# Performance work log

Measured on AMD Instinct MI355X. Metric: run time of the kernel, lower is better.

## Reference

```python
import jax, jax.numpy as jnp
import numpy as np

B = 8192
D_IN = 512
UNITS = 512


def setup_inputs() -> dict:
    key = jax.random.key(0)
    ks = jax.random.split(key, 9)
    sx = 1.0 / np.sqrt(D_IN)
    sh = 1.0 / np.sqrt(UNITS)
    return {
        "input_x": jax.random.normal(ks[0], (B, D_IN), jnp.float32),
        "input_h": jax.random.normal(ks[1], (B, UNITS), jnp.float32),
        "attention_score": jax.random.uniform(ks[2], (B, 1), jnp.float32),
        "Wx_r": jax.random.normal(ks[3], (D_IN, UNITS), jnp.float32) * sx,
        "b_r": jnp.zeros((UNITS,), jnp.float32),
        "Wh_r": jax.random.normal(ks[4], (UNITS, UNITS), jnp.float32) * sh,
        "Wx_u": jax.random.normal(ks[5], (D_IN, UNITS), jnp.float32) * sx,
        "b_u": jnp.zeros((UNITS,), jnp.float32),
        "Wh_u": jax.random.normal(ks[6], (UNITS, UNITS), jnp.float32) * sh,
        "Wx_h": jax.random.normal(ks[7], (D_IN, UNITS), jnp.float32) * sx,
        "b_h": jnp.zeros((UNITS,), jnp.float32),
        "Wh_h": jax.random.normal(ks[8], (UNITS, UNITS), jnp.float32) * sh,
    }


def reference(input_x, input_h, attention_score,
              Wx_r, b_r, Wh_r,
              Wx_u, b_u, Wh_u,
              Wx_h, b_h, Wh_h):
    # reset gate: sigmoid(Dense_b(x) + Dense(h))
    r = jax.nn.sigmoid(input_x @ Wx_r + b_r + input_h @ Wh_r)
    # update gate: sigmoid(Dense_b(x) + Dense(h))
    u = jax.nn.sigmoid(input_x @ Wx_u + b_u + input_h @ Wh_u)
    # candidate: tanh(Dense_b(x) + r * Dense(h))
    cal_h = jnp.tanh(input_x @ Wx_h + b_h + r * (input_h @ Wh_h))
    # attention-modulated update and interpolation
    u_att = attention_score * u
    h = (1.0 - u_att) * input_h + u_att * cal_h
    return h
```

## Files before the change

kernel.cpp:

```cpp
#include <hip/hip_runtime.h>
#include <hip/hip_bf16.h>

typedef __bf16 bf16x8 __attribute__((ext_vector_type(8)));
typedef float f32x4 __attribute__((ext_vector_type(4)));
typedef unsigned short us8 __attribute__((ext_vector_type(8)));

#define MFMA16 __builtin_amdgcn_mfma_f32_16x16x32_bf16

__device__ __forceinline__ unsigned short f2bf(float f) {
    unsigned int u = __float_as_uint(f);
    u += 0x7fffu + ((u >> 16) & 1u);
    return (unsigned short)(u >> 16);
}

__device__ __forceinline__ void gload_lds16(const void* g, void* l) {
    __builtin_amdgcn_global_load_lds(
        (const __attribute__((address_space(1))) unsigned int*)g,
        (__attribute__((address_space(3))) unsigned int*)l, 16, 0, 0);
}

__global__ void cvt_all_kernel(const float* __restrict__ x, const float* __restrict__ h,
                               unsigned short* __restrict__ XP, unsigned short* __restrict__ HP,
                               const float* __restrict__ W0, const float* __restrict__ W1,
                               const float* __restrict__ W2, const float* __restrict__ W3,
                               const float* __restrict__ W4, const float* __restrict__ W5,
                               unsigned short* __restrict__ WP) {
    if (blockIdx.x < 4096) {
        int c = blockIdx.x * 256 + threadIdx.x;
        const float* src = (c >> 19) ? h : x;
        unsigned short* dst = (c >> 19) ? HP : XP;
        int c2 = c & 524287;
        int mb = c2 >> 10, kb = (c2 >> 6) & 15, lane = c2 & 63;
        int r = lane & 15, ko = lane >> 4;
        const float* p = src + (size_t)(mb * 16 + r) * 512 + kb * 32 + ko * 8;
        float4 v0 = *(const float4*)p;
        float4 v1 = *(const float4*)(p + 4);
        us8 o = { f2bf(v0.x), f2bf(v0.y), f2bf(v0.z), f2bf(v0.w),
                  f2bf(v1.x), f2bf(v1.y), f2bf(v1.z), f2bf(v1.w) };
        *(us8*)(dst + (size_t)c2 * 8) = o;
    } else {
        int c = (blockIdx.x - 4096) * 256 + threadIdx.x;
        int w = c >> 15;
        const float* Wsrc;
        switch (w) {
            case 0: Wsrc = W0; break;
            case 1: Wsrc = W1; break;
            case 2: Wsrc = W2; break;
            case 3: Wsrc = W3; break;
            case 4: Wsrc = W4; break;
            default: Wsrc = W5; break;
        }
        int c2 = c & 32767;
        int nb = c2 >> 10, kb = (c2 >> 6) & 15, lane = c2 & 63;
        int cc = lane & 15, ko = lane >> 4;
        int kbase = kb * 32 + ko * 8;
        us8 o;
#pragma unroll
        for (int e = 0; e < 8; ++e)
            o[e] = f2bf(Wsrc[(size_t)(kbase + e) * 512 + nb * 16 + cc]);
        *(us8*)(WP + (size_t)c * 8) = o;
    }
}

__global__ __launch_bounds__(512, 4) void augru_mm(
    const unsigned short* __restrict__ XP,
    const unsigned short* __restrict__ HP,
    const unsigned short* __restrict__ WP,
    const float* __restrict__ b_r, const float* __restrict__ b_u, const float* __restrict__ b_h,
    const float* __restrict__ att, const float* __restrict__ h32,
    float* __restrict__ out) {
    __shared__ unsigned char sB[48 * 1024];

    const int t = threadIdx.x;
    const int wv = t >> 6, lane = t & 63;
    const int laneoff = lane * 16;

    const int bid = blockIdx.x;
    const int W = (bid & 7) * 64 + (bid >> 3);
    const int mblk = W >> 4, nblk = W & 15;
    const int wr = wv >> 1, wc = wv & 1;

    f32x4 accR[4] = {}, accU[4] = {}, accXH[4] = {}, accHH[4] = {};

    const unsigned char* XPb = (const unsigned char*)XP;
    const unsigned char* HPb = (const unsigned char*)HP;
    const unsigned char* WPb = (const unsigned char*)WP;

    size_t aoff[4];
#pragma unroll
    for (int mf = 0; mf < 4; ++mf)
        aoff[mf] = ((size_t)((mblk * 16 + wr * 4 + mf) * 16) << 10) + laneoff;

    const unsigned char* wsrc[6];
    unsigned sdst[6];
#pragma unroll
    for (int i = 0; i < 6; ++i) {
        int fid = wv + i * 8;
        int s = fid >> 3, nf = (fid >> 2) & 1, kbi = fid & 3;
        wsrc[i] = WPb + ((size_t)(s * 512 + (nblk * 2 + nf) * 16 + kbi) << 10) + laneoff;
        sdst[i] = (unsigned)fid << 10;
    }

#pragma unroll
    for (int c = 0; c < 4; ++c) {
        __syncthreads();
#pragma unroll
        for (int i = 0; i < 6; ++i)
            gload_lds16(wsrc[i] + ((size_t)c << 12), &sB[sdst[i]]);
        __syncthreads();

#pragma unroll
        for (int kbi = 0; kbi < 4; ++kbi) {
            const int kb = c * 4 + kbi;
            const size_t koff = (size_t)kb << 10;
            bf16x8 ax[4], ah[4];
#pragma unroll
            for (int mf = 0; mf < 4; ++mf) ax[mf] = *(const bf16x8*)(XPb + aoff[mf] + koff);
            const unsigned rb = (unsigned)((wc * 4 + kbi) << 10) + laneoff;
            bf16x8 b0 = *(const bf16x8*)&sB[0 * 8192 + rb];
            bf16x8 b2 = *(const bf16x8*)&sB[2 * 8192 + rb];
            bf16x8 b4 = *(const bf16x8*)&sB[4 * 8192 + rb];
#pragma unroll
            for (int mf = 0; mf < 4; ++mf) ah[mf] = *(const bf16x8*)(HPb + aoff[mf] + koff);
            __builtin_amdgcn_s_setprio(1);
#pragma unroll
            for (int mf = 0; mf < 4; ++mf) {
                accR[mf]  = MFMA16(ax[mf], b0, accR[mf], 0, 0, 0);
                accU[mf]  = MFMA16(ax[mf], b2, accU[mf], 0, 0, 0);
                accXH[mf] = MFMA16(ax[mf], b4, accXH[mf], 0, 0, 0);
            }
            __builtin_amdgcn_s_setprio(0);
            bf16x8 b1 = *(const bf16x8*)&sB[1 * 8192 + rb];
            bf16x8 b3 = *(const bf16x8*)&sB[3 * 8192 + rb];
            bf16x8 b5 = *(const bf16x8*)&sB[5 * 8192 + rb];
            __builtin_amdgcn_s_setprio(1);
#pragma unroll
            for (int mf = 0; mf < 4; ++mf) {
                accR[mf]  = MFMA16(ah[mf], b1, accR[mf], 0, 0, 0);
                accU[mf]  = MFMA16(ah[mf], b3, accU[mf], 0, 0, 0);
                accHH[mf] = MFMA16(ah[mf], b5, accHH[mf], 0, 0, 0);
            }
            __builtin_amdgcn_s_setprio(0);
        }
    }

    const int lr = lane & 15, lg = lane >> 4;
    const int col = nblk * 32 + wc * 16 + lr;
    const float br = b_r[col], bu = b_u[col], bh = b_h[col];
#pragma unroll
    for (int mf = 0; mf < 4; ++mf) {
        const int rowb = mblk * 256 + wr * 64 + mf * 16 + lg * 4;
#pragma unroll
        for (int q = 0; q < 4; ++q) {
            const int row = rowb + q;
            float r = 1.f / (1.f + __expf(-(accR[mf][q] + br)));
            float u = 1.f / (1.f + __expf(-(accU[mf][q] + bu)));
            float ph = accXH[mf][q] + bh + r * accHH[mf][q];
            ph = fminf(fmaxf(ph, -15.f), 15.f);
            float e = __expf(2.f * ph);
            float cal = (e - 1.f) / (e + 1.f);
            float hv = h32[(size_t)row * 512 + col];
            float ua = att[row] * u;
            out[(size_t)row * 512 + col] = fmaf(ua, cal - hv, hv);
        }
    }
}

extern "C" void kernel_launch(void* const* d_in, const int* in_sizes, int n_in,
                              void* d_out, int out_size, void* d_ws, size_t ws_size,
                              hipStream_t stream) {
    const float* x    = (const float*)d_in[0];
    const float* h    = (const float*)d_in[1];
    const float* att  = (const float*)d_in[2];
    const float* Wx_r = (const float*)d_in[3];
    const float* b_r  = (const float*)d_in[4];
    const float* Wh_r = (const float*)d_in[5];
    const float* Wx_u = (const float*)d_in[6];
    const float* b_u  = (const float*)d_in[7];
    const float* Wh_u = (const float*)d_in[8];
    const float* Wx_h = (const float*)d_in[9];
    const float* b_h  = (const float*)d_in[10];
    const float* Wh_h = (const float*)d_in[11];
    float* out = (float*)d_out;

    unsigned short* XP = (unsigned short*)d_ws;
    unsigned short* HP = XP + 8192 * 512;
    unsigned short* WP = HP + 8192 * 512;

    cvt_all_kernel<<<4864, 256, 0, stream>>>(x, h, XP, HP,
        Wx_r, Wh_r, Wx_u, Wh_u, Wx_h, Wh_h, WP);
    augru_mm<<<512, 512, 0, stream>>>(XP, HP, WP, b_r, b_u, b_h, att, h, out);
}
```

Baseline: 52.41 us.

## Concatenate x|h along K and double-buffer A and W tiles in LDS

The converter now packs x and h into one concatenated [B, 1024] bf16 fragment layout, and the weights into matching per-gate K-concatenated fragments. The GEMM kernel uses 256x64 output tiles instead of 256x32, so it launches 256 blocks. It stages both A and B tiles into two LDS buffers with async global-to-LDS loads and explicit vmcnt waits and barriers, replacing the previous direct global reads of A. This doubles B-fragment reuse per A load and overlaps the next tile's loads with MFMA work. In exchange it uses about 112KB of LDS and twice the accumulators per thread, which lowers occupancy, and it fills only 256 blocks.

```diff
diff --git a/kernel.cpp b/kernel.cpp
--- a/kernel.cpp
+++ b/kernel.cpp
@@ -20,15 +20,15 @@
 }
 
 __global__ void cvt_all_kernel(const float* __restrict__ x, const float* __restrict__ h,
-                               unsigned short* __restrict__ XP, unsigned short* __restrict__ HP,
+                               unsigned short* __restrict__ AP,
                                const float* __restrict__ W0, const float* __restrict__ W1,
                                const float* __restrict__ W2, const float* __restrict__ W3,
                                const float* __restrict__ W4, const float* __restrict__ W5,
                                unsigned short* __restrict__ WP) {
     if (blockIdx.x < 4096) {
         int c = blockIdx.x * 256 + threadIdx.x;
-        const float* src = (c >> 19) ? h : x;
-        unsigned short* dst = (c >> 19) ? HP : XP;
+        int ih = c >> 19;
+        const float* src = ih ? h : x;
         int c2 = c & 524287;
         int mb = c2 >> 10, kb = (c2 >> 6) & 15, lane = c2 & 63;
         int r = lane & 15, ko = lane >> 4;
@@ -37,133 +37,148 @@
         float4 v1 = *(const float4*)(p + 4);
         us8 o = { f2bf(v0.x), f2bf(v0.y), f2bf(v0.z), f2bf(v0.w),
                   f2bf(v1.x), f2bf(v1.y), f2bf(v1.z), f2bf(v1.w) };
-        *(us8*)(dst + (size_t)c2 * 8) = o;
+        *((us8*)AP + ((size_t)(mb * 32 + kb + ih * 16) << 6) + lane) = o;
     } else {
         int c = (blockIdx.x - 4096) * 256 + threadIdx.x;
-        int w = c >> 15;
+        int s = c >> 16, c2 = c & 65535;
+        int frag = c2 >> 6, lane = c2 & 63;
+        int nb = frag >> 5, kbp = frag & 31;
         const float* Wsrc;
-        switch (w) {
-            case 0: Wsrc = W0; break;
-            case 1: Wsrc = W1; break;
-            case 2: Wsrc = W2; break;
-            case 3: Wsrc = W3; break;
-            case 4: Wsrc = W4; break;
-            default: Wsrc = W5; break;
-        }
-        int c2 = c & 32767;
-        int nb = c2 >> 10, kb = (c2 >> 6) & 15, lane = c2 & 63;
+        int kb;
+        if (kbp < 16) { kb = kbp;      Wsrc = (s == 0) ? W0 : (s == 1) ? W2 : W4; }
+        else          { kb = kbp - 16; Wsrc = (s == 0) ? W1 : (s == 1) ? W3 : W5; }
         int cc = lane & 15, ko = lane >> 4;
         int kbase = kb * 32 + ko * 8;
         us8 o;
 #pragma unroll
         for (int e = 0; e < 8; ++e)
             o[e] = f2bf(Wsrc[(size_t)(kbase + e) * 512 + nb * 16 + cc]);
-        *(us8*)(WP + (size_t)c * 8) = o;
-    }
-}
-
-__global__ __launch_bounds__(512, 4) void augru_mm(
-    const unsigned short* __restrict__ XP,
-    const unsigned short* __restrict__ HP,
-    const unsigned short* __restrict__ WP,
+        *((us8*)WP + c) = o;
+    }
+}
+
+__global__ __launch_bounds__(512, 2) void augru_mm(
+    const unsigned short* __restrict__ AP_,
+    const unsigned short* __restrict__ WP_,
     const float* __restrict__ b_r, const float* __restrict__ b_u, const float* __restrict__ b_h,
     const float* __restrict__ att, const float* __restrict__ h32,
     float* __restrict__ out) {
-    __shared__ unsigned char sB[48 * 1024];
-
-    const int t = threadIdx.x;
-    const int wv = t >> 6, lane = t & 63;
+    __shared__ unsigned char sL[2][57344];
+    const unsigned char* AP  = (const unsigned char*)AP_;
+    const unsigned char* WPb = (const unsigned char*)WP_;
+
+    const int t = threadIdx.x, wv = t >> 6, lane = t & 63;
     const int laneoff = lane * 16;
 
     const int bid = blockIdx.x;
-    const int W = (bid & 7) * 64 + (bid >> 3);
-    const int mblk = W >> 4, nblk = W & 15;
+    const int Wid = (bid & 7) * 32 + (bid >> 3);
+    const int mblk = Wid >> 3, nblk = Wid & 7;
     const int wr = wv >> 1, wc = wv & 1;
 
-    f32x4 accR[4] = {}, accU[4] = {}, accXH[4] = {}, accHH[4] = {};
-
-    const unsigned char* XPb = (const unsigned char*)XP;
-    const unsigned char* HPb = (const unsigned char*)HP;
-    const unsigned char* WPb = (const unsigned char*)WP;
-
-    size_t aoff[4];
-#pragma unroll
-    for (int mf = 0; mf < 4; ++mf)
-        aoff[mf] = ((size_t)((mblk * 16 + wr * 4 + mf) * 16) << 10) + laneoff;
-
-    const unsigned char* wsrc[6];
-    unsigned sdst[6];
-#pragma unroll
-    for (int i = 0; i < 6; ++i) {
-        int fid = wv + i * 8;
-        int s = fid >> 3, nf = (fid >> 2) & 1, kbi = fid & 3;
-        wsrc[i] = WPb + ((size_t)(s * 512 + (nblk * 2 + nf) * 16 + kbi) << 10) + laneoff;
-        sdst[i] = (unsigned)fid << 10;
-    }
-
-#pragma unroll
-    for (int c = 0; c < 4; ++c) {
-        __syncthreads();
-#pragma unroll
-        for (int i = 0; i < 6; ++i)
-            gload_lds16(wsrc[i] + ((size_t)c << 12), &sB[sdst[i]]);
-        __syncthreads();
-
-#pragma unroll
-        for (int kbi = 0; kbi < 4; ++kbi) {
-            const int kb = c * 4 + kbi;
-            const size_t koff = (size_t)kb << 10;
-            bf16x8 ax[4], ah[4];
-#pragma unroll
-            for (int mf = 0; mf < 4; ++mf) ax[mf] = *(const bf16x8*)(XPb + aoff[mf] + koff);
-            const unsigned rb = (unsigned)((wc * 4 + kbi) << 10) + laneoff;
-            bf16x8 b0 = *(const bf16x8*)&sB[0 * 8192 + rb];
-            bf16x8 b2 = *(const bf16x8*)&sB[2 * 8192 + rb];
-            bf16x8 b4 = *(const bf16x8*)&sB[4 * 8192 + rb];
-#pragma unroll
-            for (int mf = 0; mf < 4; ++mf) ah[mf] = *(const bf16x8*)(HPb + aoff[mf] + koff);
-            __builtin_amdgcn_s_setprio(1);
-#pragma unroll
-            for (int mf = 0; mf < 4; ++mf) {
-                accR[mf]  = MFMA16(ax[mf], b0, accR[mf], 0, 0, 0);
-                accU[mf]  = MFMA16(ax[mf], b2, accU[mf], 0, 0, 0);
-                accXH[mf] = MFMA16(ax[mf], b4, accXH[mf], 0, 0, 0);
+    f32x4 accR[4][2] = {}, accU[4][2] = {}, accXH[4][2] = {}, accHH[4][2] = {};
+
+    const unsigned char* gsrc[7];
+    unsigned ldst[7];
+#pragma unroll
+    for (int i = 0; i < 4; ++i) {
+        int f = i * 8 + wv, mbL = f >> 1, kq = f & 1;
+        gsrc[i] = AP + ((size_t)((mblk * 16 + mbL) * 32 + kq) << 10) + laneoff;
+        ldst[i] = (unsigned)f << 10;
+    }
+#pragma unroll
+    for (int i = 4; i < 7; ++i) {
+        int g = (i - 4) * 8 + wv, s = g >> 3, nbL = (g >> 1) & 3, kq = g & 1;
+        gsrc[i] = WPb + (size_t)s * 1048576 +
+                  ((size_t)((nblk * 4 + nbL) * 32 + kq) << 10) + laneoff;
+        ldst[i] = 32768u + ((unsigned)g << 10);
+    }
+
+    unsigned aoff[4], boff[3][2];
+#pragma unroll
+    for (int mf = 0; mf < 4; ++mf) aoff[mf] = (((wr * 4 + mf) * 2) << 10) + laneoff;
+#pragma unroll
+    for (int s = 0; s < 3; ++s)
+#pragma unroll
+        for (int nf = 0; nf < 2; ++nf)
+            boff[s][nf] = 32768u + (((s * 4 + wc * 2 + nf) * 2) << 10) + laneoff;
+
+#define ISSUE(kk, bufi) { _Pragma("unroll") for (int i = 0; i < 7; ++i) \
+        gload_lds16(gsrc[i] + ((size_t)(kk) << 11), &sL[bufi][ldst[i]]); }
+
+#define WAITBAR(n) asm volatile("s_waitcnt vmcnt(" #n ")\n\ts_barrier" ::: "memory");
+#define RELBAR     asm volatile("s_waitcnt lgkmcnt(0)\n\ts_barrier" ::: "memory");
+
+#define COMPUTE(bufp, ACCC) { _Pragma("unroll") for (int kq = 0; kq < 2; ++kq) { \
+        bf16x8 ax[4]; \
+        _Pragma("unroll") for (int mf = 0; mf < 4; ++mf) \
+            ax[mf] = *(const bf16x8*)((bufp) + aoff[mf] + (kq << 10)); \
+        bf16x8 bR[2], bU[2], bC[2]; \
+        _Pragma("unroll") for (int nf = 0; nf < 2; ++nf) { \
+            bR[nf] = *(const bf16x8*)((bufp) + boff[0][nf] + (kq << 10)); \
+            bU[nf] = *(const bf16x8*)((bufp) + boff[1][nf] + (kq << 10)); \
+            bC[nf] = *(const bf16x8*)((bufp) + boff[2][nf] + (kq << 10)); } \
+        __builtin_amdgcn_s_setprio(1); \
+        _Pragma("unroll") for (int mf = 0; mf < 4; ++mf) \
+            _Pragma("unroll") for (int nf = 0; nf < 2; ++nf) { \
+                accR[mf][nf] = MFMA16(ax[mf], bR[nf], accR[mf][nf], 0, 0, 0); \
+                accU[mf][nf] = MFMA16(ax[mf], bU[nf], accU[mf][nf], 0, 0, 0); \
+                ACCC[mf][nf] = MFMA16(ax[mf], bC[nf], ACCC[mf][nf], 0, 0, 0); } \
+        __builtin_amdgcn_s_setprio(0); } }
+
+    ISSUE(0, 0)
+    ISSUE(1, 1)
+
+#pragma unroll 1
+    for (int k = 0; k < 8; ++k) {
+        unsigned char* bufp = &sL[k & 1][0];
+        WAITBAR(7)
+        COMPUTE(bufp, accXH)
+        RELBAR
+        ISSUE(k + 2, k & 1)
+    }
+#pragma unroll 1
+    for (int k = 8; k < 14; ++k) {
+        unsigned char* bufp = &sL[k & 1][0];
+        WAITBAR(7)
+        COMPUTE(bufp, accHH)
+        RELBAR
+        ISSUE(k + 2, k & 1)
+    }
+    {   unsigned char* bufp = &sL[0][0];
+        WAITBAR(7)
+        COMPUTE(bufp, accHH)
+        RELBAR }
+    {   unsigned char* bufp = &sL[1][0];
+        WAITBAR(0)
+        COMPUTE(bufp, accHH) }
+
+    const int lr = lane & 15, lg = lane >> 4;
+#pragma unroll
+    for (int nf = 0; nf < 2; ++nf) {
+        const int col = nblk * 64 + wc * 32 + nf * 16 + lr;
+        const float br = b_r[col], bu = b_u[col], bh = b_h[col];
+#pragma unroll
+        for (int mf = 0; mf < 4; ++mf) {
+            const int rowb = mblk * 256 + wr * 64 + mf * 16 + lg * 4;
+#pragma unroll
+            for (int q = 0; q < 4; ++q) {
+                const int row = rowb + q;
+                float r = 1.f / (1.f + __expf(-(accR[mf][nf][q] + br)));
+                float u = 1.f / (1.f + __expf(-(accU[mf][nf][q] + bu)));
+                float ph = accXH[mf][nf][q] + bh + r * accHH[mf][nf][q];
+                ph = fminf(fmaxf(ph, -15.f), 15.f);
+                float e = __expf(2.f * ph);
+                float cal = (e - 1.f) / (e + 1.f);
+                float hv = h32[(size_t)row * 512 + col];
+                float ua = att[row] * u;
+                out[(size_t)row * 512 + col] = fmaf(ua, cal - hv, hv);
             }
-            __builtin_amdgcn_s_setprio(0);
-            bf16x8 b1 = *(const bf16x8*)&sB[1 * 8192 + rb];
-            bf16x8 b3 = *(const bf16x8*)&sB[3 * 8192 + rb];
-            bf16x8 b5 = *(const bf16x8*)&sB[5 * 8192 + rb];
-            __builtin_amdgcn_s_setprio(1);
-#pragma unroll
-            for (int mf = 0; mf < 4; ++mf) {
-                accR[mf]  = MFMA16(ah[mf], b1, accR[mf], 0, 0, 0);
-                accU[mf]  = MFMA16(ah[mf], b3, accU[mf], 0, 0, 0);
-                accHH[mf] = MFMA16(ah[mf], b5, accHH[mf], 0, 0, 0);
-            }
-            __builtin_amdgcn_s_setprio(0);
         }
     }
-
-    const int lr = lane & 15, lg = lane >> 4;
-    const int col = nblk * 32 + wc * 16 + lr;
-    const float br = b_r[col], bu = b_u[col], bh = b_h[col];
-#pragma unroll
-    for (int mf = 0; mf < 4; ++mf) {
-        const int rowb = mblk * 256 + wr * 64 + mf * 16 + lg * 4;
-#pragma unroll
-        for (int q = 0; q < 4; ++q) {
-            const int row = rowb + q;
-            float r = 1.f / (1.f + __expf(-(accR[mf][q] + br)));
-            float u = 1.f / (1.f + __expf(-(accU[mf][q] + bu)));
-            float ph = accXH[mf][q] + bh + r * accHH[mf][q];
-            ph = fminf(fmaxf(ph, -15.f), 15.f);
-            float e = __expf(2.f * ph);
-            float cal = (e - 1.f) / (e + 1.f);
-            float hv = h32[(size_t)row * 512 + col];
-            float ua = att[row] * u;
-            out[(size_t)row * 512 + col] = fmaf(ua, cal - hv, hv);
-        }
-    }
+#undef ISSUE
+#undef WAITBAR
+#undef RELBAR
+#undef COMPUTE
 }
 
 extern "C" void kernel_launch(void* const* d_in, const int* in_sizes, int n_in,
@@ -183,11 +198,10 @@
     const float* Wh_h = (const float*)d_in[11];
     float* out = (float*)d_out;
 
-    unsigned short* XP = (unsigned short*)d_ws;
-    unsigned short* HP = XP + 8192 * 512;
-    unsigned short* WP = HP + 8192 * 512;
-
-    cvt_all_kernel<<<4864, 256, 0, stream>>>(x, h, XP, HP,
+    unsigned short* AP = (unsigned short*)d_ws;
+    unsigned short* WP = AP + 8388608;
+
+    cvt_all_kernel<<<4864, 256, 0, stream>>>(x, h, AP,
         Wx_r, Wh_r, Wx_u, Wh_u, Wx_h, Wh_h, WP);
-    augru_mm<<<512, 512, 0, stream>>>(XP, HP, WP, b_r, b_u, b_h, att, h, out);
-}
+    augru_mm<<<256, 512, 0, stream>>>(AP, WP, b_r, b_u, b_h, att, h, out);
+}
```

New measurement: 45.94 us. -12.3%, faster.
